# Kernel tuning notes

Hardware: AMD Instinct MI355X
Metric: run time of the kernel (lower is better)

The kernel has to match this reference:

```python
import jax, jax.numpy as jnp
import numpy as np


def setup_inputs() -> dict:
    key = jax.random.key(0)
    k1, k2 = jax.random.split(key)
    B, Ld, Lq, D = 32, 2048, 512, 256
    doc = jax.random.normal(k1, (B, Ld, D), dtype=jnp.float32)
    query = jax.random.normal(k2, (B, Lq, D), dtype=jnp.float32)
    doc_mask = jnp.ones((B, Ld), dtype=jnp.float32)
    q_mask = jnp.ones((B, Lq), dtype=jnp.float32)
    return {"doc": doc, "query": query, "doc_mask": doc_mask, "q_mask": q_mask}


def reference(doc, query, doc_mask, q_mask):
    # match_score: [B, Lq, Ld] = tanh(query @ doc^T)
    match_score = jnp.tanh(jnp.einsum('bqd,btd->bqt', query, doc))
    # sum over query positions -> [B, Ld]; softmax over doc positions
    query_to_doc_att = jax.nn.softmax(jnp.sum(match_score, axis=1), axis=-1)
    # sum over doc positions -> [B, Lq]; softmax over query positions
    doc_to_query_att = jax.nn.softmax(jnp.sum(match_score, axis=-1), axis=-1)
    # mask and renormalize
    alpha = query_to_doc_att * doc_mask
    alpha = alpha / jnp.sum(alpha, axis=1, keepdims=True)
    beta = doc_to_query_att * q_mask
    beta = beta / jnp.sum(beta, axis=1, keepdims=True)
    # weighted pooling: doc^T @ alpha -> [B, D]; query^T @ beta -> [B, D]
    doc_vector = jnp.einsum('btd,bt->bd', doc, alpha)
    que_vector = jnp.einsum('bqd,bq->bd', query, beta)
    return jnp.concatenate([doc_vector, que_vector], axis=1)  # [B, 2D]
```

## Files before the change

kernel.cpp:

```cpp
#include <hip/hip_runtime.h>
#include <hip/hip_bf16.h>
#include <cstdint>

#define BB 32
#define LD 2048
#define LQ 512
#define DD 256
#define BM 128
#define BN 128
#define BK 32

typedef _Float16 half8 __attribute__((ext_vector_type(8)));
typedef _Float16 half4 __attribute__((ext_vector_type(4)));
typedef float float4v __attribute__((ext_vector_type(4)));

__device__ __forceinline__ float tanh_fast(float x) {
    float e = __expf(2.0f * x);
    return 1.0f - 2.0f / (e + 1.0f);
}

__device__ __forceinline__ void load_lds16(const void* g, void* s) {
    __builtin_amdgcn_global_load_lds((const __attribute__((address_space(1))) void*)g,
                                     (__attribute__((address_space(3))) void*)s, 16, 0, 0);
}

__global__ __launch_bounds__(256) void kconv(const float* __restrict__ src,
                                             _Float16* __restrict__ dst, int n8) {
    int i = blockIdx.x * 256 + threadIdx.x;
    if (i >= n8) return;
    const float4v* s = (const float4v*)src + (size_t)i * 2;
    float4v a = s[0], c = s[1];
    half8 h = {(_Float16)a[0], (_Float16)a[1], (_Float16)a[2], (_Float16)a[3],
               (_Float16)c[0], (_Float16)c[1], (_Float16)c[2], (_Float16)c[3]};
    *((half8*)dst + i) = h;
}

template <bool F16SRC>
__global__ __launch_bounds__(256, 2) void k1(const void* __restrict__ qsrc,
                                             const void* __restrict__ dsrc,
                                             float* __restrict__ alog,
                                             float* __restrict__ blog) {
    __shared__ _Float16 sQ[BM * BK];
    __shared__ _Float16 sD[BN * BK];
    const int bq = blockIdx.x, bt = blockIdx.y, b = blockIdx.z;
    const int tid = threadIdx.x;
    const int lane = tid & 63;
    const int wave = tid >> 6;
    const int r16 = lane & 15;
    const int q4 = lane >> 4;
    const int mb = (wave >> 1) * 64, nb = (wave & 1) * 64;

    float4v acc[4][4];
    float4v zero = {0.f, 0.f, 0.f, 0.f};
#pragma unroll
    for (int m = 0; m < 4; m++)
#pragma unroll
        for (int n = 0; n < 4; n++) acc[m][n] = zero;

    for (int kk = 0; kk < DD; kk += BK) {
        __syncthreads();
        if constexpr (F16SRC) {
            const _Float16* Qh = (const _Float16*)qsrc + ((size_t)b * LQ + bq * BM) * DD;
            const _Float16* Dh = (const _Float16*)dsrc + ((size_t)b * LD + bt * BN) * DD;
#pragma unroll
            for (int j = 0; j < 2; j++) {
                int c = 2 * wave + j;
                int row = 16 * c + (lane >> 2);
                int col = (lane & 3) * 8;
                load_lds16(Qh + (size_t)row * DD + kk + col, &sQ[c * 512]);
                load_lds16(Dh + (size_t)row * DD + kk + col, &sD[c * 512]);
            }
        } else {
            const float* Qf = (const float*)qsrc + ((size_t)b * LQ + bq * BM) * DD;
            const float* Df = (const float*)dsrc + ((size_t)b * LD + bt * BN) * DD;
#pragma unroll
            for (int i = 0; i < 4; i++) {
                int f = tid + 256 * i;
                int row = f >> 3, c = f & 7;
                float4v v = *(const float4v*)(Qf + (size_t)row * DD + kk + 4 * c);
                half4 h = {(_Float16)v[0], (_Float16)v[1], (_Float16)v[2], (_Float16)v[3]};
                *(half4*)(&sQ[row * BK + 4 * c]) = h;
                float4v w = *(const float4v*)(Df + (size_t)row * DD + kk + 4 * c);
                half4 h2 = {(_Float16)w[0], (_Float16)w[1], (_Float16)w[2], (_Float16)w[3]};
                *(half4*)(&sD[row * BK + 4 * c]) = h2;
            }
        }
        __syncthreads();

        half8 af[4], bf[4];
#pragma unroll
        for (int m = 0; m < 4; m++) af[m] = *(const half8*)(&sQ[(mb + 16 * m + r16) * BK + 8 * q4]);
#pragma unroll
        for (int n = 0; n < 4; n++) bf[n] = *(const half8*)(&sD[(nb + 16 * n + r16) * BK + 8 * q4]);
#pragma unroll
        for (int m = 0; m < 4; m++)
#pragma unroll
            for (int n = 0; n < 4; n++)
                acc[m][n] = __builtin_amdgcn_mfma_f32_16x16x32_f16(af[m], bf[n], acc[m][n], 0, 0, 0);
    }

    float rsum[4][4];
    float csum[4];
#pragma unroll
    for (int m = 0; m < 4; m++)
#pragma unroll
        for (int r = 0; r < 4; r++) rsum[m][r] = 0.f;
#pragma unroll
    for (int n = 0; n < 4; n++) csum[n] = 0.f;

#pragma unroll
    for (int m = 0; m < 4; m++)
#pragma unroll
        for (int n = 0; n < 4; n++) {
            float t0 = tanh_fast(acc[m][n][0]);
            float t1 = tanh_fast(acc[m][n][1]);
            float t2 = tanh_fast(acc[m][n][2]);
            float t3 = tanh_fast(acc[m][n][3]);
            csum[n] += t0 + t1 + t2 + t3;
            rsum[m][0] += t0;
            rsum[m][1] += t1;
            rsum[m][2] += t2;
            rsum[m][3] += t3;
        }

#pragma unroll
    for (int m = 0; m < 4; m++) {
#pragma unroll
        for (int r = 0; r < 4; r++) {
            float v = rsum[m][r];
            v += __shfl_xor(v, 1);
            v += __shfl_xor(v, 2);
            v += __shfl_xor(v, 4);
            v += __shfl_xor(v, 8);
            rsum[m][r] = v;
        }
        if (r16 < 4) {
            float v = (r16 == 0) ? rsum[m][0] : (r16 == 1) ? rsum[m][1] : (r16 == 2) ? rsum[m][2] : rsum[m][3];
            atomicAdd(blog + b * LQ + bq * BM + mb + 16 * m + 4 * q4 + r16, v);
        }
    }
#pragma unroll
    for (int n = 0; n < 4; n++) {
        float v = csum[n];
        v += __shfl_xor(v, 16);
        v += __shfl_xor(v, 32);
        if (lane < 16) atomicAdd(alog + b * LD + bt * BN + nb + 16 * n + lane, v);
    }
}

__global__ __launch_bounds__(256) void k2(const float* __restrict__ alog, const float* __restrict__ blog,
                                          const float* __restrict__ dmask, const float* __restrict__ qmask,
                                          float* __restrict__ alpha, float* __restrict__ beta) {
    int blk = blockIdx.x;
    const float *lg, *mk;
    float* out;
    int n;
    if (blk < BB) {
        lg = alog + blk * LD; mk = dmask + blk * LD; out = alpha + blk * LD; n = LD;
    } else {
        int b = blk - BB;
        lg = blog + b * LQ; mk = qmask + b * LQ; out = beta + b * LQ; n = LQ;
    }
    int tid = threadIdx.x, lane = tid & 63, wave = tid >> 6;
    __shared__ float sm[4], ss[4];
    float mx = -3.0e38f;
    for (int i = tid; i < n; i += 256) mx = fmaxf(mx, lg[i]);
#pragma unroll
    for (int s = 1; s < 64; s <<= 1) mx = fmaxf(mx, __shfl_xor(mx, s));
    if (lane == 0) sm[wave] = mx;
    __syncthreads();
    mx = fmaxf(fmaxf(sm[0], sm[1]), fmaxf(sm[2], sm[3]));
    float sum = 0.f;
    for (int i = tid; i < n; i += 256) sum += __expf(lg[i] - mx) * mk[i];
#pragma unroll
    for (int s = 1; s < 64; s <<= 1) sum += __shfl_xor(sum, s);
    if (lane == 0) ss[wave] = sum;
    __syncthreads();
    sum = ss[0] + ss[1] + ss[2] + ss[3];
    float inv = 1.0f / sum;
    for (int i = tid; i < n; i += 256) out[i] = __expf(lg[i] - mx) * mk[i] * inv;
}

template <bool F16SRC>
__global__ __launch_bounds__(256) void k3(const float* __restrict__ docf, const float* __restrict__ qryf,
                                          const _Float16* __restrict__ dh, const _Float16* __restrict__ qh,
                                          const float* __restrict__ alpha, const float* __restrict__ beta,
                                          float* __restrict__ out) {
    int blk = blockIdx.x, d = threadIdx.x;
    if (blk < BB * 16) {
        int b = blk >> 4, ch = blk & 15;
        const float* w = alpha + b * LD + ch * 128;
        size_t base = ((size_t)b * LD + ch * 128) * DD + d;
        float acc = 0.f;
        for (int t = 0; t < 128; t++) {
            float x = F16SRC ? (float)dh[base + (size_t)t * DD] : docf[base + (size_t)t * DD];
            acc += w[t] * x;
        }
        atomicAdd(out + b * 2 * DD + d, acc);
    } else {
        int bk2 = blk - BB * 16;
        int b = bk2 >> 2, ch = bk2 & 3;
        const float* w = beta + b * LQ + ch * 128;
        size_t base = ((size_t)b * LQ + ch * 128) * DD + d;
        float acc = 0.f;
        for (int t = 0; t < 128; t++) {
            float x = F16SRC ? (float)qh[base + (size_t)t * DD] : qryf[base + (size_t)t * DD];
            acc += w[t] * x;
        }
        atomicAdd(out + b * 2 * DD + DD + d, acc);
    }
}

extern "C" void kernel_launch(void* const* d_in, const int* in_sizes, int n_in,
                              void* d_out, int out_size, void* d_ws, size_t ws_size,
                              hipStream_t stream) {
    (void)in_sizes; (void)n_in; (void)out_size;
    const float* doc = (const float*)d_in[0];
    const float* qry = (const float*)d_in[1];
    const float* dmask = (const float*)d_in[2];
    const float* qmask = (const float*)d_in[3];
    float* out = (float*)d_out;

    float* alog = (float*)d_ws;
    float* blog = alog + BB * LD;
    float* alpha = blog + BB * LQ;
    float* beta = alpha + BB * LD;
    _Float16* dh = (_Float16*)(beta + BB * LQ);
    _Float16* qh = dh + (size_t)BB * LD * DD;
    size_t needed = (size_t)(2 * BB * LD + 2 * BB * LQ) * 4 +
                    ((size_t)BB * LD * DD + (size_t)BB * LQ * DD) * 2;
    bool useF16 = ws_size >= needed;

    hipMemsetAsync(alog, 0, (size_t)(BB * LD + BB * LQ) * 4, stream);
    hipMemsetAsync(d_out, 0, (size_t)BB * 2 * DD * 4, stream);

    if (useF16) {
        kconv<<<(BB * LD * DD / 8 + 255) / 256, 256, 0, stream>>>(doc, dh, BB * LD * DD / 8);
        kconv<<<(BB * LQ * DD / 8 + 255) / 256, 256, 0, stream>>>(qry, qh, BB * LQ * DD / 8);
        k1<true><<<dim3(LQ / BM, LD / BN, BB), 256, 0, stream>>>(qh, dh, alog, blog);
    } else {
        k1<false><<<dim3(LQ / BM, LD / BN, BB), 256, 0, stream>>>(qry, doc, alog, blog);
    }
    k2<<<2 * BB, 256, 0, stream>>>(alog, blog, dmask, qmask, alpha, beta);
    if (useF16) {
        k3<true><<<BB * 16 + BB * 4, 256, 0, stream>>>(doc, qry, dh, qh, alpha, beta, out);
    } else {
        k3<false><<<BB * 16 + BB * 4, 256, 0, stream>>>(doc, qry, dh, qh, alpha, beta, out);
    }
}
```

Measured before the change: 171.8 us.

## Double K tile with swizzled LDS, merge conversion kernels, vectorize pooling

Raises the GEMM K tile from 32 to 64 and adds an XOR swizzle to the LDS layout, which halves the barrier/load iterations and aims to avoid bank conflicts on fragment reads. The occupancy hint on the launch bounds is dropped. The two fp16 conversion launches are merged into one kernel, and the pooling kernel now reads half8 vectors per thread with an LDS reduction instead of scalar strided loads. The risks are higher LDS use per block, which can lower occupancy, and the added cost of the shared-memory reduction.

```diff
diff --git a/kernel.cpp b/kernel.cpp
--- a/kernel.cpp
+++ b/kernel.cpp
@@ -8,7 +8,7 @@
 #define DD 256
 #define BM 128
 #define BN 128
-#define BK 32
+#define BK 64
 
 typedef _Float16 half8 __attribute__((ext_vector_type(8)));
 typedef _Float16 half4 __attribute__((ext_vector_type(4)));
@@ -24,22 +24,31 @@
                                      (__attribute__((address_space(3))) void*)s, 16, 0, 0);
 }
 
-__global__ __launch_bounds__(256) void kconv(const float* __restrict__ src,
-                                             _Float16* __restrict__ dst, int n8) {
+#define DOCN8 (BB * LD * DD / 8)
+#define QRYN8 (BB * LQ * DD / 8)
+
+__global__ __launch_bounds__(256) void kconv(const float* __restrict__ doc,
+                                             const float* __restrict__ qry,
+                                             _Float16* __restrict__ dh,
+                                             _Float16* __restrict__ qh) {
     int i = blockIdx.x * 256 + threadIdx.x;
-    if (i >= n8) return;
-    const float4v* s = (const float4v*)src + (size_t)i * 2;
+    const float* src;
+    _Float16* dst;
+    int idx;
+    if (i < DOCN8) { src = doc; dst = dh; idx = i; }
+    else           { src = qry; dst = qh; idx = i - DOCN8; }
+    const float4v* s = (const float4v*)src + (size_t)idx * 2;
     float4v a = s[0], c = s[1];
     half8 h = {(_Float16)a[0], (_Float16)a[1], (_Float16)a[2], (_Float16)a[3],
                (_Float16)c[0], (_Float16)c[1], (_Float16)c[2], (_Float16)c[3]};
-    *((half8*)dst + i) = h;
+    *((half8*)dst + idx) = h;
 }
 
 template <bool F16SRC>
-__global__ __launch_bounds__(256, 2) void k1(const void* __restrict__ qsrc,
-                                             const void* __restrict__ dsrc,
-                                             float* __restrict__ alog,
-                                             float* __restrict__ blog) {
+__global__ __launch_bounds__(256) void k1(const void* __restrict__ qsrc,
+                                          const void* __restrict__ dsrc,
+                                          float* __restrict__ alog,
+                                          float* __restrict__ blog) {
     __shared__ _Float16 sQ[BM * BK];
     __shared__ _Float16 sD[BN * BK];
     const int bq = blockIdx.x, bt = blockIdx.y, b = blockIdx.z;
@@ -57,46 +66,54 @@
 #pragma unroll
         for (int n = 0; n < 4; n++) acc[m][n] = zero;
 
+    const int lrow = lane >> 3;
+    const int lcol = ((lane & 7) ^ lrow) * 8;
+
     for (int kk = 0; kk < DD; kk += BK) {
         __syncthreads();
         if constexpr (F16SRC) {
             const _Float16* Qh = (const _Float16*)qsrc + ((size_t)b * LQ + bq * BM) * DD;
             const _Float16* Dh = (const _Float16*)dsrc + ((size_t)b * LD + bt * BN) * DD;
 #pragma unroll
-            for (int j = 0; j < 2; j++) {
-                int c = 2 * wave + j;
-                int row = 16 * c + (lane >> 2);
-                int col = (lane & 3) * 8;
-                load_lds16(Qh + (size_t)row * DD + kk + col, &sQ[c * 512]);
-                load_lds16(Dh + (size_t)row * DD + kk + col, &sD[c * 512]);
+            for (int j = 0; j < 4; j++) {
+                int c = wave * 4 + j;
+                int row = 8 * c + lrow;
+                load_lds16(Qh + (size_t)row * DD + kk + lcol, &sQ[c * 512]);
+                load_lds16(Dh + (size_t)row * DD + kk + lcol, &sD[c * 512]);
             }
         } else {
             const float* Qf = (const float*)qsrc + ((size_t)b * LQ + bq * BM) * DD;
             const float* Df = (const float*)dsrc + ((size_t)b * LD + bt * BN) * DD;
 #pragma unroll
-            for (int i = 0; i < 4; i++) {
+            for (int i = 0; i < 8; i++) {
                 int f = tid + 256 * i;
-                int row = f >> 3, c = f & 7;
+                int row = f >> 4, c = f & 15;
+                int c2 = c >> 1, hlf = c & 1;
+                int p = c2 ^ (row & 7);
                 float4v v = *(const float4v*)(Qf + (size_t)row * DD + kk + 4 * c);
                 half4 h = {(_Float16)v[0], (_Float16)v[1], (_Float16)v[2], (_Float16)v[3]};
-                *(half4*)(&sQ[row * BK + 4 * c]) = h;
+                *(half4*)(&sQ[row * BK + p * 8 + hlf * 4]) = h;
                 float4v w = *(const float4v*)(Df + (size_t)row * DD + kk + 4 * c);
                 half4 h2 = {(_Float16)w[0], (_Float16)w[1], (_Float16)w[2], (_Float16)w[3]};
-                *(half4*)(&sD[row * BK + 4 * c]) = h2;
+                *(half4*)(&sD[row * BK + p * 8 + hlf * 4]) = h2;
             }
         }
         __syncthreads();
 
-        half8 af[4], bf[4];
-#pragma unroll
-        for (int m = 0; m < 4; m++) af[m] = *(const half8*)(&sQ[(mb + 16 * m + r16) * BK + 8 * q4]);
-#pragma unroll
-        for (int n = 0; n < 4; n++) bf[n] = *(const half8*)(&sD[(nb + 16 * n + r16) * BK + 8 * q4]);
-#pragma unroll
-        for (int m = 0; m < 4; m++)
-#pragma unroll
-            for (int n = 0; n < 4; n++)
-                acc[m][n] = __builtin_amdgcn_mfma_f32_16x16x32_f16(af[m], bf[n], acc[m][n], 0, 0, 0);
+#pragma unroll
+        for (int kk2 = 0; kk2 < 2; kk2++) {
+            const int sw = ((4 * kk2 + q4) ^ (r16 & 7)) * 8;
+            half8 af[4], bf[4];
+#pragma unroll
+            for (int m = 0; m < 4; m++) af[m] = *(const half8*)(&sQ[(mb + 16 * m + r16) * BK + sw]);
+#pragma unroll
+            for (int n = 0; n < 4; n++) bf[n] = *(const half8*)(&sD[(nb + 16 * n + r16) * BK + sw]);
+#pragma unroll
+            for (int m = 0; m < 4; m++)
+#pragma unroll
+                for (int n = 0; n < 4; n++)
+                    acc[m][n] = __builtin_amdgcn_mfma_f32_16x16x32_f16(af[m], bf[n], acc[m][n], 0, 0, 0);
+        }
     }
 
     float rsum[4][4];
@@ -186,29 +203,51 @@
                                           const _Float16* __restrict__ dh, const _Float16* __restrict__ qh,
                                           const float* __restrict__ alpha, const float* __restrict__ beta,
                                           float* __restrict__ out) {
-    int blk = blockIdx.x, d = threadIdx.x;
+    __shared__ float sm[8 * DD];
+    int blk = blockIdx.x, tid = threadIdx.x;
+    const _Float16* srch;
+    const float* srcf;
+    const float* w;
+    float* dst;
     if (blk < BB * 16) {
         int b = blk >> 4, ch = blk & 15;
-        const float* w = alpha + b * LD + ch * 128;
-        size_t base = ((size_t)b * LD + ch * 128) * DD + d;
-        float acc = 0.f;
-        for (int t = 0; t < 128; t++) {
-            float x = F16SRC ? (float)dh[base + (size_t)t * DD] : docf[base + (size_t)t * DD];
-            acc += w[t] * x;
-        }
-        atomicAdd(out + b * 2 * DD + d, acc);
-    } else {
-        int bk2 = blk - BB * 16;
-        int b = bk2 >> 2, ch = bk2 & 3;
-        const float* w = beta + b * LQ + ch * 128;
-        size_t base = ((size_t)b * LQ + ch * 128) * DD + d;
-        float acc = 0.f;
-        for (int t = 0; t < 128; t++) {
-            float x = F16SRC ? (float)qh[base + (size_t)t * DD] : qryf[base + (size_t)t * DD];
-            acc += w[t] * x;
-        }
-        atomicAdd(out + b * 2 * DD + DD + d, acc);
-    }
+        srch = dh + ((size_t)b * LD + ch * 128) * DD;
+        srcf = docf + ((size_t)b * LD + ch * 128) * DD;
+        w = alpha + b * LD + ch * 128;
+        dst = out + b * 2 * DD;
+    } else {
+        int k = blk - BB * 16;
+        int b = k >> 2, ch = k & 3;
+        srch = qh + ((size_t)b * LQ + ch * 128) * DD;
+        srcf = qryf + ((size_t)b * LQ + ch * 128) * DD;
+        w = beta + b * LQ + ch * 128;
+        dst = out + b * 2 * DD + DD;
+    }
+    int g = tid >> 5, c = tid & 31;
+    float acc[8];
+#pragma unroll
+    for (int j = 0; j < 8; j++) acc[j] = 0.f;
+    for (int r = 0; r < 16; r++) {
+        int t = r * 8 + g;
+        float wt = w[t];
+        if constexpr (F16SRC) {
+            half8 x = *(const half8*)(srch + (size_t)t * DD + c * 8);
+#pragma unroll
+            for (int j = 0; j < 8; j++) acc[j] += wt * (float)x[j];
+        } else {
+            const float4v* p = (const float4v*)(srcf + (size_t)t * DD + c * 8);
+            float4v x0 = p[0], x1 = p[1];
+#pragma unroll
+            for (int j = 0; j < 4; j++) { acc[j] += wt * x0[j]; acc[4 + j] += wt * x1[j]; }
+        }
+    }
+#pragma unroll
+    for (int j = 0; j < 8; j++) sm[g * DD + c * 8 + j] = acc[j];
+    __syncthreads();
+    float s = 0.f;
+#pragma unroll
+    for (int g2 = 0; g2 < 8; g2++) s += sm[g2 * DD + tid];
+    atomicAdd(dst + tid, s);
 }
 
 extern "C" void kernel_launch(void* const* d_in, const int* in_sizes, int n_in,
@@ -235,8 +274,7 @@
     hipMemsetAsync(d_out, 0, (size_t)BB * 2 * DD * 4, stream);
 
     if (useF16) {
-        kconv<<<(BB * LD * DD / 8 + 255) / 256, 256, 0, stream>>>(doc, dh, BB * LD * DD / 8);
-        kconv<<<(BB * LQ * DD / 8 + 255) / 256, 256, 0, stream>>>(qry, qh, BB * LQ * DD / 8);
+        kconv<<<(DOCN8 + QRYN8) / 256, 256, 0, stream>>>(doc, qry, dh, qh);
         k1<true><<<dim3(LQ / BM, LD / BN, BB), 256, 0, stream>>>(qh, dh, alog, blog);
     } else {
         k1<false><<<dim3(LQ / BM, LD / BN, BB), 256, 0, stream>>>(qry, doc, alog, blog);
```

Measured after the change: 169.1 us. Within noise of the previous version (-1.6%).
